# Kernel tuning notes

Measured on AMD Instinct MI355X. Metric: run time of the kernel, lower is better.

## Reference

```python
import jax, jax.numpy as jnp
import numpy as np

B, C, Wd, Ht = 16, 256, 64, 64
C2 = C // 2

def setup_inputs() -> dict:
    key = jax.random.key(0)
    ks = jax.random.split(key, 9)
    s = 0.05  # keep logits in a sane range (d_qk=128)
    return {
        "x": jax.random.normal(ks[0], (B, C, Wd, Ht), jnp.float32),
        "y": jax.random.normal(ks[1], (B, C, Wd, Ht), jnp.float32),
        "Wq": jax.random.normal(ks[2], (C2, C), jnp.float32) * s,
        "bq": jax.random.normal(ks[3], (C2,), jnp.float32) * s,
        "Wk": jax.random.normal(ks[4], (C2, C), jnp.float32) * s,
        "bk": jax.random.normal(ks[5], (C2,), jnp.float32) * s,
        "Wv": jax.random.normal(ks[6], (C, C), jnp.float32) * s,
        "bv": jax.random.normal(ks[7], (C,), jnp.float32) * s,
        "gamma": jax.random.normal(ks[8], (1,), jnp.float32),
    }

def reference(x, y, Wq, bq, Wk, bk, Wv, bv, gamma):
    b, c, w, h = x.shape
    n = w * h
    xf = x.reshape(b, c, n)           # (B, C, N)
    yf = y.reshape(b, c, n)           # (B, C, N)
    # conv1x1 == channel matmul
    q = jnp.einsum('oc,bcn->bno', Wq, xf) + bq                    # (B, N, C2)
    k = jnp.einsum('oc,bcn->bon', Wk, yf) + bk[None, :, None]     # (B, C2, N)
    energy = jnp.einsum('bno,bom->bnm', q, k)                     # (B, N, N)
    attn = jax.nn.softmax(energy, axis=-1)
    v = jnp.einsum('oc,bcn->bon', Wv, yf) + bv[None, :, None]     # (B, C, N)
    out = jnp.einsum('bon,bmn->bom', v, attn)                     # V @ attn^T
    out = out.reshape(b, c, w, h)
    return gamma[0] * out + y
```

## Files before the change

### kernel.cpp

```cpp
#include <hip/hip_runtime.h>
#include <stdint.h>

using f32x4  = __attribute__((ext_vector_type(4))) float;
using f32x16 = __attribute__((ext_vector_type(16))) float;
using f16x8  = __attribute__((ext_vector_type(8))) _Float16;

#define NB  16
#define NC  256
#define NC2 128
#define NN  4096
#define TILE_B 49152

__device__ __forceinline__ unsigned int pk2(float a, float b) {
    auto h = __builtin_amdgcn_cvt_pkrtz(a, b);
    return __builtin_bit_cast(unsigned int, h);
}

__device__ __forceinline__ f16x8 pack8(f32x4 a, f32x4 b) {
    union { unsigned int w[4]; f16x8 v; } u;
    u.w[0] = pk2(a[0], a[1]); u.w[1] = pk2(a[2], a[3]);
    u.w[2] = pk2(b[0], b[1]); u.w[3] = pk2(b[2], b[3]);
    return u.v;
}

__device__ __forceinline__ void gload16(const void* g, void* l) {
    __builtin_amdgcn_global_load_lds(
        (const __attribute__((address_space(1))) unsigned int*)g,
        (__attribute__((address_space(3))) unsigned int*)l, 16, 0, 0);
}

__global__ __launch_bounds__(256, 2) void qkv_kernel(
    const float* __restrict__ x, const float* __restrict__ y,
    const float* __restrict__ Wq, const float* __restrict__ bq,
    const float* __restrict__ Wk, const float* __restrict__ bk,
    const float* __restrict__ Wv, const float* __restrict__ bv,
    unsigned short* __restrict__ Qf, char* __restrict__ KV)
{
    __shared__ __align__(16) char lds[65536];

    const int bid   = blockIdx.x;
    const int ntile = bid & 63;
    const int bb    = bid >> 6;
    const int nblk  = ntile * 64;

    const int t    = threadIdx.x;
    const int lane = t & 63;
    const int wid  = t >> 6;
    const int l31  = lane & 31;
    const int s    = lane >> 5;

    {
        const bool isQ = (wid < 2);
        const float* srcb = (isQ ? x : y) + (size_t)bb * NC * NN;
        const float* W    = isQ ? Wq : Wk;
        const float* bias = isQ ? bq : bk;
        const int wo = (wid & 1) * 64;
        const int base = isQ ? 49152 : 0;

        f32x16 acc[2][2];
        #pragma unroll
        for (int a = 0; a < 2; ++a)
            #pragma unroll
            for (int bc = 0; bc < 2; ++bc) acc[a][bc] = (f32x16)(0.0f);

        #pragma unroll 4
        for (int ks = 0; ks < 16; ++ks) {
            const int c0 = ks * 16 + s * 8;
            f16x8 wf[2], xf[2];
            #pragma unroll
            for (int a = 0; a < 2; ++a) {
                const float* wr = W + (size_t)(wo + a * 32 + l31) * NC + c0;
                wf[a] = pack8(*(const f32x4*)wr, *(const f32x4*)(wr + 4));
            }
            #pragma unroll
            for (int bc = 0; bc < 2; ++bc) {
                const float* xc = srcb + (size_t)c0 * NN + nblk + bc * 32 + l31;
                f32x4 v0, v1;
                v0[0] = xc[0*NN]; v0[1] = xc[1*NN]; v0[2] = xc[2*NN]; v0[3] = xc[3*NN];
                v1[0] = xc[4*NN]; v1[1] = xc[5*NN]; v1[2] = xc[6*NN]; v1[3] = xc[7*NN];
                xf[bc] = pack8(v0, v1);
            }
            #pragma unroll
            for (int a = 0; a < 2; ++a)
                #pragma unroll
                for (int bc = 0; bc < 2; ++bc)
                    acc[a][bc] = __builtin_amdgcn_mfma_f32_32x32x16_f16(
                        wf[a], xf[bc], acc[a][bc], 0, 0, 0);
        }

        #pragma unroll
        for (int a = 0; a < 2; ++a) {
            #pragma unroll
            for (int bc = 0; bc < 2; ++bc) {
                const int nr = bc * 32 + l31;
                #pragma unroll
                for (int g = 0; g < 4; ++g) {
                    const int o0 = wo + a * 32 + 8 * g + 4 * s;
                    const f32x4 bv4 = *(const f32x4*)(bias + o0);
                    union { unsigned int w[2]; uint2 u2; } pk;
                    pk.w[0] = pk2(acc[a][bc][g*4+0] + bv4[0], acc[a][bc][g*4+1] + bv4[1]);
                    pk.w[1] = pk2(acc[a][bc][g*4+2] + bv4[2], acc[a][bc][g*4+3] + bv4[3]);
                    const int dst = base + nr*256 +
                        (((o0 >> 3) << 4) ^ ((nr & 7) << 4)) + (o0 & 7) * 2;
                    *(uint2*)(lds + dst) = pk.u2;
                }
            }
        }
    }

    {
        const float* srcb = y + (size_t)bb * NC * NN;
        const int wo = wid * 64;

        f32x16 acc[2][2];
        #pragma unroll
        for (int a = 0; a < 2; ++a)
            #pragma unroll
            for (int bc = 0; bc < 2; ++bc) acc[a][bc] = (f32x16)(0.0f);

        #pragma unroll 4
        for (int ks = 0; ks < 16; ++ks) {
            const int c0 = ks * 16 + s * 8;
            f16x8 wf[2], xf[2];
            #pragma unroll
            for (int a = 0; a < 2; ++a) {
                const float* wr = Wv + (size_t)(wo + a * 32 + l31) * NC + c0;
                wf[a] = pack8(*(const f32x4*)wr, *(const f32x4*)(wr + 4));
            }
            #pragma unroll
            for (int bc = 0; bc < 2; ++bc) {
                const float* xc = srcb + (size_t)c0 * NN + nblk + bc * 32 + l31;
                f32x4 v0, v1;
                v0[0] = xc[0*NN]; v0[1] = xc[1*NN]; v0[2] = xc[2*NN]; v0[3] = xc[3*NN];
                v1[0] = xc[4*NN]; v1[1] = xc[5*NN]; v1[2] = xc[6*NN]; v1[3] = xc[7*NN];
                xf[bc] = pack8(v0, v1);
            }
            #pragma unroll
            for (int a = 0; a < 2; ++a)
                #pragma unroll
                for (int bc = 0; bc < 2; ++bc)
                    acc[a][bc] = __builtin_amdgcn_mfma_f32_32x32x16_f16(
                        xf[bc], wf[a], acc[a][bc], 0, 0, 0);
        }

        #pragma unroll
        for (int a = 0; a < 2; ++a) {
            const int o = wo + a * 32 + l31;
            const float bvo = bv[o];
            #pragma unroll
            for (int bc = 0; bc < 2; ++bc) {
                #pragma unroll
                for (int g = 0; g < 4; ++g) {
                    const int nr = bc * 32 + 8 * g + 4 * s;
                    union { unsigned int w[2]; uint2 u2; } pk;
                    pk.w[0] = pk2(acc[a][bc][g*4+0] + bvo, acc[a][bc][g*4+1] + bvo);
                    pk.w[1] = pk2(acc[a][bc][g*4+2] + bvo, acc[a][bc][g*4+3] + bvo);
                    const int dst = 16384 + o*128 +
                        (((nr >> 3) << 4) ^ ((o & 7) << 4)) + (nr & 7) * 2;
                    *(uint2*)(lds + dst) = pk.u2;
                }
            }
        }
    }

    __syncthreads();

    char* kvt = KV + (size_t)(bb*64 + ntile) * TILE_B;
    #pragma unroll
    for (int i = 0; i < 12; ++i) {
        const int off = (i*256 + t) * 16;
        *(uint4*)(kvt + off) = *(const uint4*)(lds + off);
    }
    char* qg = (char*)Qf + ((size_t)(bb*NN + nblk)) * NC2 * 2;
    #pragma unroll
    for (int i = 0; i < 4; ++i) {
        const int g = (i*256 + t) * 16;
        const int sidx = 49152 + (g ^ (((g >> 8) & 7) << 4));
        *(uint4*)(qg + g) = *(const uint4*)(lds + sidx);
    }
}

__global__ __launch_bounds__(256, 2) void attn_kernel(
    const unsigned short* __restrict__ Qf, const char* __restrict__ KV,
    const float* __restrict__ yg, const float* __restrict__ gamma,
    float* __restrict__ outp)
{
    __shared__ __align__(16) char tile[TILE_B];

    const int bid = ((blockIdx.x & 7) << 6) + (blockIdx.x >> 3);
    const int bb = bid >> 5;
    const int m0 = (bid & 31) * 128;
    const int t    = threadIdx.x;
    const int lane = t & 63;
    const int wv   = t >> 6;
    const int qcol = lane & 31;
    const int s    = lane >> 5;

    f16x8 qf[8];
    {
        const char* qrow = (const char*)Qf +
            (((size_t)bb*NN + m0 + wv*32 + qcol) * NC2) * 2;
        #pragma unroll
        for (int ks = 0; ks < 8; ++ks)
            qf[ks] = *(const f16x8*)(qrow + ks*32 + s*16);
    }

    f32x16 acc[8];
    #pragma unroll
    for (int ob = 0; ob < 8; ++ob) acc[ob] = (f32x16)(0.0f);
    float m_run = -3.0e38f, l_run = 0.0f;

    const char* kvb = KV + (size_t)bb * 64 * TILE_B;

    #pragma unroll
    for (int i = 0; i < 12; ++i)
        gload16(kvb + ((i*256 + t) << 4), tile + ((i*256 + wv*64) << 4));

    #pragma unroll 1
    for (int it = 0; it < 64; ++it) {
        asm volatile("s_waitcnt vmcnt(0)" ::: "memory");
        __syncthreads();

        #pragma unroll
        for (int kb = 0; kb < 2; ++kb) {
            f32x16 sS = (f32x16)(0.0f);
            const int key = kb*32 + qcol;
            const int rb  = key*256;
            const int sw  = (key&7) << 4;
            #pragma unroll
            for (int ks = 0; ks < 8; ++ks) {
                f16x8 kf = *(const f16x8*)(tile + rb + ((ks*32 + s*16) ^ sw));
                sS = __builtin_amdgcn_mfma_f32_32x32x16_f16(kf, qf[ks], sS, 0, 0, 0);
            }

            float pmax = fmaxf(fmaxf(fmaxf(sS[0], sS[1]), fmaxf(sS[2], sS[3])),
                               fmaxf(fmaxf(sS[4], sS[5]), fmaxf(sS[6], sS[7])));
            pmax = fmaxf(pmax,
                   fmaxf(fmaxf(fmaxf(sS[8], sS[9]), fmaxf(sS[10], sS[11])),
                         fmaxf(fmaxf(sS[12], sS[13]), fmaxf(sS[14], sS[15]))));
            pmax = fmaxf(pmax, __shfl_xor(pmax, 32));
            if (__any(pmax > m_run + 8.0f)) {
                const float mn = fmaxf(m_run, pmax);
                const float sc = __expf(m_run - mn);
                m_run = mn; l_run *= sc;
                #pragma unroll
                for (int ob = 0; ob < 8; ++ob)
                    #pragma unroll
                    for (int r = 0; r < 16; ++r) acc[ob][r] *= sc;
            }
            float p[16];
            float rs = 0.f;
            #pragma unroll
            for (int r = 0; r < 16; ++r) {
                p[r] = __expf(sS[r] - m_run);
                rs += p[r];
            }
            rs += __shfl_xor(rs, 32);
            l_run += rs;

            f16x8 pb0, pb1;
            #pragma unroll
            for (int ks2 = 0; ks2 < 2; ++ks2) {
                unsigned int pA0, pA1, pB0, pB1;
                if (ks2 == 0) {
                    pA0 = pk2(p[0], p[1]);  pA1 = pk2(p[2], p[3]);
                    pB0 = pk2(p[4], p[5]);  pB1 = pk2(p[6], p[7]);
                } else {
                    pA0 = pk2(p[8], p[9]);  pA1 = pk2(p[10], p[11]);
                    pB0 = pk2(p[12], p[13]); pB1 = pk2(p[14], p[15]);
                }
                const unsigned int lv0 = s ? pB0 : pA0;
                const unsigned int lv1 = s ? pB1 : pA1;
                const unsigned int sd0 = s ? pA0 : pB0;
                const unsigned int sd1 = s ? pA1 : pB1;
                const unsigned int rv0 = (unsigned int)__shfl_xor((int)sd0, 32);
                const unsigned int rv1 = (unsigned int)__shfl_xor((int)sd1, 32);
                union { unsigned int w[4]; f16x8 v; } u;
                u.w[0] = s ? rv0 : lv0;
                u.w[1] = s ? rv1 : lv1;
                u.w[2] = s ? lv0 : rv0;
                u.w[3] = s ? lv1 : rv1;
                if (ks2 == 0) pb0 = u.v; else pb1 = u.v;
            }

            #pragma unroll
            for (int ks2 = 0; ks2 < 2; ++ks2) {
                const int colb = kb*64 + ks2*32 + s*16;
                const f16x8 pbx = ks2 ? pb1 : pb0;
                #pragma unroll
                for (int ob = 0; ob < 8; ++ob) {
                    const int o = ob*32 + qcol;
                    f16x8 vf = *(const f16x8*)(tile + 16384 + o*128 +
                                               (colb ^ ((o&7)<<4)));
                    acc[ob] = __builtin_amdgcn_mfma_f32_32x32x16_f16(vf, pbx, acc[ob], 0, 0, 0);
                }
            }
        }

        __syncthreads();
        if (it < 63) {
            const char* src = kvb + (size_t)(it+1) * TILE_B;
            #pragma unroll
            for (int i = 0; i < 12; ++i)
                gload16(src + ((i*256 + t) << 4), tile + ((i*256 + wv*64) << 4));
        }
    }

    const float ga   = gamma[0];
    const float invl = 1.0f / l_run;
    const int n = m0 + wv*32 + qcol;
    #pragma unroll
    for (int ob = 0; ob < 8; ++ob) {
        #pragma unroll
        for (int r = 0; r < 16; ++r) {
            const int o = ob*32 + (r&3) + 8*(r>>2) + 4*s;
            const size_t a = ((size_t)(bb*NC + o))*NN + n;
            outp[a] = fmaf(acc[ob][r]*invl, ga, yg[a]);
        }
    }
}

extern "C" void kernel_launch(void* const* d_in, const int* in_sizes, int n_in,
                              void* d_out, int out_size, void* d_ws, size_t ws_size,
                              hipStream_t stream) {
    (void)in_sizes; (void)n_in; (void)out_size; (void)ws_size;
    const float* x     = (const float*)d_in[0];
    const float* y     = (const float*)d_in[1];
    const float* Wq    = (const float*)d_in[2];
    const float* bq    = (const float*)d_in[3];
    const float* Wk    = (const float*)d_in[4];
    const float* bk    = (const float*)d_in[5];
    const float* Wv    = (const float*)d_in[6];
    const float* bv    = (const float*)d_in[7];
    const float* gamma = (const float*)d_in[8];
    float* out = (float*)d_out;

    unsigned short* Qf = (unsigned short*)d_ws;
    char* KV = (char*)(Qf + (size_t)NB*NN*NC2);

    qkv_kernel<<<dim3(1024), dim3(256), 0, stream>>>(
        x, y, Wq, bq, Wk, bk, Wv, bv, Qf, KV);
    attn_kernel<<<dim3(512), dim3(256), 0, stream>>>(
        Qf, KV, y, gamma, out);
}
```

Baseline: 319.6 us.

## Double-buffer K tiles and overlap V/K loads with attention compute

Splits the shared tile into a double-buffered K region and a single V region. The next K tile is prefetched while the current tile's softmax runs, and the next V tile is loaded after the PV matmuls, using partial vmcnt waits and raw s_barriers in place of a full drain and __syncthreads. It also widens the K/Q LDS XOR swizzle from 8 to 16 rows to reduce bank conflicts, processes both 32-key halves' QK before the softmax, and raises wave priority around the MFMA sections. The cost is more LDS (64KB versus 48KB), which may limit the two-blocks-per-CU occupancy, plus fragile hand-counted vmcnt bookkeeping.

```diff
diff --git a/kernel.cpp b/kernel.cpp
--- a/kernel.cpp
+++ b/kernel.cpp
@@ -101,7 +101,7 @@
                     pk.w[0] = pk2(acc[a][bc][g*4+0] + bv4[0], acc[a][bc][g*4+1] + bv4[1]);
                     pk.w[1] = pk2(acc[a][bc][g*4+2] + bv4[2], acc[a][bc][g*4+3] + bv4[3]);
                     const int dst = base + nr*256 +
-                        (((o0 >> 3) << 4) ^ ((nr & 7) << 4)) + (o0 & 7) * 2;
+                        (((o0 >> 3) << 4) ^ ((nr & 15) << 4)) + (o0 & 7) * 2;
                     *(uint2*)(lds + dst) = pk.u2;
                 }
             }
@@ -175,7 +175,7 @@
     #pragma unroll
     for (int i = 0; i < 4; ++i) {
         const int g = (i*256 + t) * 16;
-        const int sidx = 49152 + (g ^ (((g >> 8) & 7) << 4));
+        const int sidx = 49152 + (g ^ (((g >> 8) & 15) << 4));
         *(uint4*)(qg + g) = *(const uint4*)(lds + sidx);
     }
 }
@@ -185,7 +185,8 @@
     const float* __restrict__ yg, const float* __restrict__ gamma,
     float* __restrict__ outp)
 {
-    __shared__ __align__(16) char tile[TILE_B];
+    __shared__ __align__(16) char kls[2][16384];
+    __shared__ __align__(16) char vls[32768];
 
     const int bid = ((blockIdx.x & 7) << 6) + (blockIdx.x >> 3);
     const int bb = bid >> 5;
@@ -213,31 +214,54 @@
     const char* kvb = KV + (size_t)bb * 64 * TILE_B;
 
     #pragma unroll
-    for (int i = 0; i < 12; ++i)
-        gload16(kvb + ((i*256 + t) << 4), tile + ((i*256 + wv*64) << 4));
+    for (int i = 0; i < 4; ++i)
+        gload16(kvb + ((i*256 + t) << 4), kls[0] + ((i*256 + wv*64) << 4));
+    #pragma unroll
+    for (int i = 0; i < 8; ++i)
+        gload16(kvb + 16384 + ((i*256 + t) << 4), vls + ((i*256 + wv*64) << 4));
 
     #pragma unroll 1
     for (int it = 0; it < 64; ++it) {
-        asm volatile("s_waitcnt vmcnt(0)" ::: "memory");
-        __syncthreads();
-
-        #pragma unroll
-        for (int kb = 0; kb < 2; ++kb) {
-            f32x16 sS = (f32x16)(0.0f);
-            const int key = kb*32 + qcol;
-            const int rb  = key*256;
-            const int sw  = (key&7) << 4;
+        asm volatile("s_waitcnt vmcnt(8)" ::: "memory");
+        __builtin_amdgcn_s_barrier();
+        asm volatile("" ::: "memory");
+
+        const char* kbuf = kls[it & 1];
+        const char* nsrc = kvb + (size_t)((it + 1) & 63) * TILE_B;
+
+        f32x16 sA = (f32x16)(0.0f), sB = (f32x16)(0.0f);
+        {
+            const int keyA = qcol, keyB = 32 + qcol;
+            const int rbA = keyA * 256, rbB = keyB * 256;
+            const int swA = (keyA & 15) << 4, swB = (keyB & 15) << 4;
+            __builtin_amdgcn_s_setprio(1);
             #pragma unroll
             for (int ks = 0; ks < 8; ++ks) {
-                f16x8 kf = *(const f16x8*)(tile + rb + ((ks*32 + s*16) ^ sw));
-                sS = __builtin_amdgcn_mfma_f32_32x32x16_f16(kf, qf[ks], sS, 0, 0, 0);
-            }
-
-            float pmax = fmaxf(fmaxf(fmaxf(sS[0], sS[1]), fmaxf(sS[2], sS[3])),
-                               fmaxf(fmaxf(sS[4], sS[5]), fmaxf(sS[6], sS[7])));
-            pmax = fmaxf(pmax,
-                   fmaxf(fmaxf(fmaxf(sS[8], sS[9]), fmaxf(sS[10], sS[11])),
-                         fmaxf(fmaxf(sS[12], sS[13]), fmaxf(sS[14], sS[15]))));
+                f16x8 kf = *(const f16x8*)(kbuf + rbA + ((ks*32 + s*16) ^ swA));
+                sA = __builtin_amdgcn_mfma_f32_32x32x16_f16(kf, qf[ks], sA, 0, 0, 0);
+            }
+            #pragma unroll
+            for (int ks = 0; ks < 8; ++ks) {
+                f16x8 kf = *(const f16x8*)(kbuf + rbB + ((ks*32 + s*16) ^ swB));
+                sB = __builtin_amdgcn_mfma_f32_32x32x16_f16(kf, qf[ks], sB, 0, 0, 0);
+            }
+            __builtin_amdgcn_s_setprio(0);
+        }
+
+        {
+            char* kdst = (char*)kls[(it + 1) & 1];
+            #pragma unroll
+            for (int i = 0; i < 4; ++i)
+                gload16(nsrc + ((i*256 + t) << 4), kdst + ((i*256 + wv*64) << 4));
+        }
+
+        f16x8 pfr[2][2];
+        {
+            float pmax = -3.0e38f;
+            #pragma unroll
+            for (int r = 0; r < 16; ++r) pmax = fmaxf(pmax, sA[r]);
+            #pragma unroll
+            for (int r = 0; r < 16; ++r) pmax = fmaxf(pmax, sB[r]);
             pmax = fmaxf(pmax, __shfl_xor(pmax, 32));
             if (__any(pmax > m_run + 8.0f)) {
                 const float mn = fmaxf(m_run, pmax);
@@ -248,63 +272,83 @@
                     #pragma unroll
                     for (int r = 0; r < 16; ++r) acc[ob][r] *= sc;
             }
-            float p[16];
+            float pa[16], pb[16];
             float rs = 0.f;
             #pragma unroll
-            for (int r = 0; r < 16; ++r) {
-                p[r] = __expf(sS[r] - m_run);
-                rs += p[r];
-            }
+            for (int r = 0; r < 16; ++r) { pa[r] = __expf(sA[r] - m_run); rs += pa[r]; }
+            #pragma unroll
+            for (int r = 0; r < 16; ++r) { pb[r] = __expf(sB[r] - m_run); rs += pb[r]; }
             rs += __shfl_xor(rs, 32);
             l_run += rs;
 
-            f16x8 pb0, pb1;
-            #pragma unroll
-            for (int ks2 = 0; ks2 < 2; ++ks2) {
-                unsigned int pA0, pA1, pB0, pB1;
-                if (ks2 == 0) {
-                    pA0 = pk2(p[0], p[1]);  pA1 = pk2(p[2], p[3]);
-                    pB0 = pk2(p[4], p[5]);  pB1 = pk2(p[6], p[7]);
-                } else {
-                    pA0 = pk2(p[8], p[9]);  pA1 = pk2(p[10], p[11]);
-                    pB0 = pk2(p[12], p[13]); pB1 = pk2(p[14], p[15]);
+            #pragma unroll
+            for (int kb = 0; kb < 2; ++kb) {
+                #pragma unroll
+                for (int ks2 = 0; ks2 < 2; ++ks2) {
+                    unsigned int pA0, pA1, pB0, pB1;
+                    if (kb == 0) {
+                        if (ks2 == 0) {
+                            pA0 = pk2(pa[0], pa[1]);  pA1 = pk2(pa[2], pa[3]);
+                            pB0 = pk2(pa[4], pa[5]);  pB1 = pk2(pa[6], pa[7]);
+                        } else {
+                            pA0 = pk2(pa[8], pa[9]);  pA1 = pk2(pa[10], pa[11]);
+                            pB0 = pk2(pa[12], pa[13]); pB1 = pk2(pa[14], pa[15]);
+                        }
+                    } else {
+                        if (ks2 == 0) {
+                            pA0 = pk2(pb[0], pb[1]);  pA1 = pk2(pb[2], pb[3]);
+                            pB0 = pk2(pb[4], pb[5]);  pB1 = pk2(pb[6], pb[7]);
+                        } else {
+                            pA0 = pk2(pb[8], pb[9]);  pA1 = pk2(pb[10], pb[11]);
+                            pB0 = pk2(pb[12], pb[13]); pB1 = pk2(pb[14], pb[15]);
+                        }
+                    }
+                    const unsigned int lv0 = s ? pB0 : pA0;
+                    const unsigned int lv1 = s ? pB1 : pA1;
+                    const unsigned int sd0 = s ? pA0 : pB0;
+                    const unsigned int sd1 = s ? pA1 : pB1;
+                    const unsigned int rv0 = (unsigned int)__shfl_xor((int)sd0, 32);
+                    const unsigned int rv1 = (unsigned int)__shfl_xor((int)sd1, 32);
+                    union { unsigned int w[4]; f16x8 v; } u;
+                    u.w[0] = s ? rv0 : lv0;
+                    u.w[1] = s ? rv1 : lv1;
+                    u.w[2] = s ? lv0 : rv0;
+                    u.w[3] = s ? lv1 : rv1;
+                    pfr[kb][ks2] = u.v;
                 }
-                const unsigned int lv0 = s ? pB0 : pA0;
-                const unsigned int lv1 = s ? pB1 : pA1;
-                const unsigned int sd0 = s ? pA0 : pB0;
-                const unsigned int sd1 = s ? pA1 : pB1;
-                const unsigned int rv0 = (unsigned int)__shfl_xor((int)sd0, 32);
-                const unsigned int rv1 = (unsigned int)__shfl_xor((int)sd1, 32);
-                union { unsigned int w[4]; f16x8 v; } u;
-                u.w[0] = s ? rv0 : lv0;
-                u.w[1] = s ? rv1 : lv1;
-                u.w[2] = s ? lv0 : rv0;
-                u.w[3] = s ? lv1 : rv1;
-                if (ks2 == 0) pb0 = u.v; else pb1 = u.v;
-            }
-
+            }
+        }
+
+        asm volatile("s_waitcnt vmcnt(4)" ::: "memory");
+        __builtin_amdgcn_s_barrier();
+        asm volatile("" ::: "memory");
+
+        __builtin_amdgcn_s_setprio(1);
+        #pragma unroll
+        for (int kb = 0; kb < 2; ++kb) {
             #pragma unroll
             for (int ks2 = 0; ks2 < 2; ++ks2) {
                 const int colb = kb*64 + ks2*32 + s*16;
-                const f16x8 pbx = ks2 ? pb1 : pb0;
+                const f16x8 pbx = pfr[kb][ks2];
                 #pragma unroll
                 for (int ob = 0; ob < 8; ++ob) {
                     const int o = ob*32 + qcol;
-                    f16x8 vf = *(const f16x8*)(tile + 16384 + o*128 +
-                                               (colb ^ ((o&7)<<4)));
+                    f16x8 vf = *(const f16x8*)(vls + o*128 + (colb ^ ((o&7)<<4)));
                     acc[ob] = __builtin_amdgcn_mfma_f32_32x32x16_f16(vf, pbx, acc[ob], 0, 0, 0);
                 }
             }
         }
-
-        __syncthreads();
-        if (it < 63) {
-            const char* src = kvb + (size_t)(it+1) * TILE_B;
-            #pragma unroll
-            for (int i = 0; i < 12; ++i)
-                gload16(src + ((i*256 + t) << 4), tile + ((i*256 + wv*64) << 4));
-        }
-    }
+        __builtin_amdgcn_s_setprio(0);
+
+        asm volatile("" ::: "memory");
+        __builtin_amdgcn_s_barrier();
+        asm volatile("" ::: "memory");
+
+        #pragma unroll
+        for (int i = 0; i < 8; ++i)
+            gload16(nsrc + 16384 + ((i*256 + t) << 4), vls + ((i*256 + wv*64) << 4));
+    }
+    asm volatile("s_waitcnt vmcnt(0)" ::: "memory");
 
     const float ga   = gamma[0];
     const float invl = 1.0f / l_run;
```

Result: faster. 306.1 us (-4.2%).
